# Kernel tuning notes

Hardware: AMD Instinct MI355X
Metric: run time of the kernel (lower is better)

The kernel has to match this reference:

```python
import jax, jax.numpy as jnp
import numpy as np

# dims: B batch, R seq_num (MSA rows), L seq_len (residues), D emb_dim, C n_emb_2D, H heads
B, R, L, D, C, H = 1, 256, 384, 512, 256, 4
HD = D // H
SCALE = np.float32((HD ** -0.5) / np.sqrt(L))  # head-dim scaling * seqlen_scaling (1/sqrt(L))
EPS = 1e-5


def setup_inputs() -> dict:
    key = jax.random.key(0)
    ks = jax.random.split(key, 6)
    s = 0.02
    return {
        "x": jax.random.normal(ks[0], (B, R, L, D), jnp.float32),
        "pair_feat": jax.random.normal(ks[1], (B, L, L, C), jnp.float32),
        "attn_mask": jnp.ones((B, L), jnp.int32),
        "ln_msa_g": jnp.ones((D,), jnp.float32),
        "ln_msa_b": jnp.zeros((D,), jnp.float32),
        "ln_pair_g": jnp.ones((C,), jnp.float32),
        "ln_pair_b": jnp.zeros((C,), jnp.float32),
        "W_pair": jax.random.normal(ks[2], (C, H), jnp.float32) * s,  # stacked per-head [C,1] linears
        "W_v": jax.random.normal(ks[3], (D, D), jnp.float32) * s,     # stacked per-head [D,HD] value proj
        "W_out": jax.random.normal(ks[4], (D, D), jnp.float32) * s,   # to_out (bias=False)
    }


def _ln(x, g, b):
    mu = jnp.mean(x, axis=-1, keepdims=True)
    var = jnp.mean(jnp.square(x - mu), axis=-1, keepdims=True)
    return (x - mu) * jax.lax.rsqrt(var + EPS) * g + b


def reference(x, pair_feat, attn_mask, ln_msa_g, ln_msa_b, ln_pair_g, ln_pair_b, W_pair, W_v, W_out):
    # MHPair_to_MSA.forward (eval mode, dropout=0)
    msa = _ln(x, ln_msa_g, ln_msa_b)                                  # [B,R,L,D]
    pf = (pair_feat + jnp.swapaxes(pair_feat, 1, 2)) * 0.5            # symmetrize
    pf = _ln(pf, ln_pair_g, ln_pair_b)                                # [B,L,L,C]
    # pair-feature-derived attention logits (no QK^T)
    logits = jnp.einsum('bijc,ch->bhij', pf * SCALE, W_pair)          # [B,H,L,L]
    V = jnp.einsum('brld,de->brle', msa, W_v).reshape(B, R, L, H, HD) # [B,R,L,H,HD]
    mask2 = attn_mask[:, :, None] * attn_mask[:, None, :]             # [B,L,L]
    logits = jnp.where(mask2[:, None, :, :] == 0,
                       jnp.finfo(logits.dtype).min, logits)
    attn = jax.nn.softmax(logits, axis=-1)                            # [B,H,L,L]
    out = jnp.einsum('bhij,brjhd->brihd', attn, V).reshape(B, R, L, D)
    out = out @ W_out                                                 # to_out, bias=False
    return x + out                                                    # residual
```

## Files before the change

kernel.cpp:

```cpp
#include <hip/hip_runtime.h>

#define L_   384
#define D_   512
#define C_   256
#define H_   4
#define RR_  256
#define M1_  98304
#define LL2_ 147456
#define NPAIR_BLOCKS 18480
#define NLN_BLOCKS 24576

typedef __bf16 bf16x8 __attribute__((ext_vector_type(8)));
typedef float f32x4 __attribute__((ext_vector_type(4)));

__device__ __forceinline__ unsigned short f2bf_bits(float f) {
  union { float f; unsigned u; } v; v.f = f;
  return (unsigned short)((v.u + 0x7fffu + ((v.u >> 16) & 1u)) >> 16);
}
__device__ __forceinline__ __bf16 f2bf(float f) {
  union { unsigned short s; __bf16 b; } o; o.s = f2bf_bits(f);
  return o.b;
}

__global__ __launch_bounds__(256) void ln_wtrans_kernel(
    const float* __restrict__ x, const float* __restrict__ g,
    const float* __restrict__ b, __bf16* __restrict__ msa,
    const float* __restrict__ Wv, const float* __restrict__ Wo,
    __bf16* __restrict__ WvT, __bf16* __restrict__ WoT) {
  if (blockIdx.x < NLN_BLOCKS) {
    int row = blockIdx.x * 4 + (threadIdx.x >> 6);
    int lane = threadIdx.x & 63;
    const float4* xr = (const float4*)(x + (size_t)row * D_ + lane * 8);
    float4 v0 = xr[0], v1 = xr[1];
    float s1 = v0.x + v0.y + v0.z + v0.w + v1.x + v1.y + v1.z + v1.w;
    float s2 = v0.x * v0.x + v0.y * v0.y + v0.z * v0.z + v0.w * v0.w +
               v1.x * v1.x + v1.y * v1.y + v1.z * v1.z + v1.w * v1.w;
#pragma unroll
    for (int o = 32; o > 0; o >>= 1) {
      s1 += __shfl_xor(s1, o);
      s2 += __shfl_xor(s2, o);
    }
    float mu = s1 * (1.0f / D_);
    float var = s2 * (1.0f / D_) - mu * mu;
    float rs = rsqrtf(var + 1e-5f);
    const float4* gp = (const float4*)(g + lane * 8);
    const float4* bp = (const float4*)(b + lane * 8);
    float4 g0 = gp[0], g1 = gp[1], b0 = bp[0], b1 = bp[1];
    float y[8];
    y[0] = (v0.x - mu) * rs * g0.x + b0.x;
    y[1] = (v0.y - mu) * rs * g0.y + b0.y;
    y[2] = (v0.z - mu) * rs * g0.z + b0.z;
    y[3] = (v0.w - mu) * rs * g0.w + b0.w;
    y[4] = (v1.x - mu) * rs * g1.x + b1.x;
    y[5] = (v1.y - mu) * rs * g1.y + b1.y;
    y[6] = (v1.z - mu) * rs * g1.z + b1.z;
    y[7] = (v1.w - mu) * rs * g1.w + b1.w;
    uint4 pk;
    pk.x = ((unsigned)f2bf_bits(y[1]) << 16) | f2bf_bits(y[0]);
    pk.y = ((unsigned)f2bf_bits(y[3]) << 16) | f2bf_bits(y[2]);
    pk.z = ((unsigned)f2bf_bits(y[5]) << 16) | f2bf_bits(y[4]);
    pk.w = ((unsigned)f2bf_bits(y[7]) << 16) | f2bf_bits(y[6]);
    *(uint4*)(msa + (size_t)row * D_ + lane * 8) = pk;
  } else {
    int id = (blockIdx.x - NLN_BLOCKS) * 256 + threadIdx.x;
    int m = id >> 18;
    int e = (id >> 9) & 511, d = id & 511;
    const float* W = m ? Wo : Wv;
    __bf16* T = m ? WoT : WvT;
    T[(size_t)e * 512 + d] = f2bf(W[(size_t)d * 512 + e]);
  }
}

__global__ __launch_bounds__(256) void pair_logits_kernel(
    const float* __restrict__ pf, const int* __restrict__ mask,
    const float* __restrict__ g, const float* __restrict__ b,
    const float* __restrict__ Wp, float* __restrict__ logits) {
  unsigned wid = blockIdx.x * 4 + (threadIdx.x >> 6);
  int lane = threadIdx.x & 63;
  unsigned a = wid / 385u;
  unsigned c = wid - a * 385u;
  int i, j;
  if (c < 384u - a) { i = a; j = a + c; }
  else { i = 383 - a; j = i + (c - (384 - a)); }

  int c0 = lane * 4;
  float4 p1 = *(const float4*)(pf + ((size_t)i * L_ + j) * C_ + c0);
  float4 p2 = *(const float4*)(pf + ((size_t)j * L_ + i) * C_ + c0);
  float4 v;
  v.x = 0.5f * (p1.x + p2.x); v.y = 0.5f * (p1.y + p2.y);
  v.z = 0.5f * (p1.z + p2.z); v.w = 0.5f * (p1.w + p2.w);
  float s1 = v.x + v.y + v.z + v.w;
  float s2 = v.x * v.x + v.y * v.y + v.z * v.z + v.w * v.w;
#pragma unroll
  for (int o = 32; o > 0; o >>= 1) {
    s1 += __shfl_xor(s1, o);
    s2 += __shfl_xor(s2, o);
  }
  float mu = s1 * (1.0f / C_);
  float var = s2 * (1.0f / C_) - mu * mu;
  float rs = rsqrtf(var + 1e-5f);
  float4 gv = *(const float4*)(g + c0);
  float4 bv = *(const float4*)(b + c0);
  float y0 = (v.x - mu) * rs * gv.x + bv.x;
  float y1 = (v.y - mu) * rs * gv.y + bv.y;
  float y2 = (v.z - mu) * rs * gv.z + bv.z;
  float y3 = (v.w - mu) * rs * gv.w + bv.w;
  const float4* wp = (const float4*)Wp;
  float4 w0 = wp[c0], w1 = wp[c0 + 1], w2 = wp[c0 + 2], w3 = wp[c0 + 3];
  float4 t;
  t.x = y0 * w0.x + y1 * w1.x + y2 * w2.x + y3 * w3.x;
  t.y = y0 * w0.y + y1 * w1.y + y2 * w2.y + y3 * w3.y;
  t.z = y0 * w0.z + y1 * w1.z + y2 * w2.z + y3 * w3.z;
  t.w = y0 * w0.w + y1 * w1.w + y2 * w2.w + y3 * w3.w;
#pragma unroll
  for (int o = 32; o > 0; o >>= 1) {
    t.x += __shfl_xor(t.x, o);
    t.y += __shfl_xor(t.y, o);
    t.z += __shfl_xor(t.z, o);
    t.w += __shfl_xor(t.w, o);
  }
  if (lane < 8) {
    int h = lane & 3;
    int ii = (lane < 4) ? i : j;
    int jj = (lane < 4) ? j : i;
    bool ok = (mask[i] != 0) && (mask[j] != 0);
    const float NEG = -3.402823466e38f;
    const float SCALE = (float)(0.08838834764831845 / 19.595917942265423);
    float th = (h == 0) ? t.x : (h == 1) ? t.y : (h == 2) ? t.z : t.w;
    logits[(size_t)h * LL2_ + (size_t)ii * L_ + jj] = ok ? SCALE * th : NEG;
  }
}

__global__ __launch_bounds__(256) void softmax_kernel(
    const float* __restrict__ logits, __bf16* __restrict__ attn) {
  int wave = threadIdx.x >> 6, lane = threadIdx.x & 63;
  int row = blockIdx.x * 4 + wave;
  const float* lr = logits + (size_t)row * L_;
  float v[6];
#pragma unroll
  for (int t = 0; t < 6; ++t) v[t] = lr[lane + t * 64];
  float mx = v[0];
#pragma unroll
  for (int t = 1; t < 6; ++t) mx = fmaxf(mx, v[t]);
#pragma unroll
  for (int o = 32; o > 0; o >>= 1) mx = fmaxf(mx, __shfl_xor(mx, o));
  float s = 0.f;
#pragma unroll
  for (int t = 0; t < 6; ++t) { v[t] = __expf(v[t] - mx); s += v[t]; }
#pragma unroll
  for (int o = 32; o > 0; o >>= 1) s += __shfl_xor(s, o);
  float inv = 1.0f / s;
  __bf16* ar = attn + (size_t)row * L_;
#pragma unroll
  for (int t = 0; t < 6; ++t) ar[lane + t * 64] = f2bf(v[t] * inv);
}

__device__ __forceinline__ void gload16(const void* g, void* l) {
  __builtin_amdgcn_global_load_lds(
      (const __attribute__((address_space(1))) void*)g,
      (__attribute__((address_space(3))) void*)l, 16, 0, 0);
}

__device__ __forceinline__ unsigned xcd_swz_3072(unsigned bid) {
  return (bid & 7u) * 384u + (bid >> 3);
}
__device__ __forceinline__ unsigned xcd_swz_768(unsigned bid) {
  return (bid & 7u) * 96u + (bid >> 3);
}

template <int NT>
__device__ __forceinline__ void stage_part32(__bf16* s, const __bf16* g, size_t ld) {
  int tid = threadIdx.x;
#pragma unroll
  for (int i = 0; i < 2; ++i) {
    int cid = i * NT + tid;
    int row = cid >> 2, c = cid & 3;
    int cs = c ^ ((row >> 1) & 3);
    gload16(g + (size_t)row * ld + cs * 8, (char*)s + cid * 16);
  }
}

__device__ __forceinline__ bf16x8 frag_ld32(const __bf16* s, int row, int fk) {
  int c = (fk >> 3) ^ ((row >> 1) & 3);
  return *(const bf16x8*)((const char*)s + row * 64 + c * 16);
}

__device__ __forceinline__ void mainloop256_2s(
    const __bf16* __restrict__ A, size_t ldA,
    const __bf16* __restrict__ B, size_t ldB,
    int K, __bf16* lds, f32x4 acc[8][4]) {
  int lane = threadIdx.x & 63, wave = threadIdx.x >> 6;
  int wm = (wave >> 2) * 128, wn = (wave & 3) * 64;
  int fr = lane & 15, fk = (lane >> 4) * 8;
  int nt = K >> 5;
  const int SLOT = 512 * 32;
  stage_part32<512>(lds, A, ldA);
  stage_part32<512>(lds + 256 * 32, B, ldB);
  for (int t = 0; t < nt; ++t) {
    const __bf16* As = lds + (t & 1) * SLOT;
    const __bf16* Bs = As + 256 * 32;
    if (t + 1 < nt) {
      __bf16* d = lds + ((t + 1) & 1) * SLOT;
      stage_part32<512>(d, A + (size_t)(t + 1) * 32, ldA);
      stage_part32<512>(d + 256 * 32, B + (size_t)(t + 1) * 32, ldB);
      asm volatile("s_waitcnt vmcnt(4)" ::: "memory");
    } else {
      asm volatile("s_waitcnt vmcnt(0)" ::: "memory");
    }
    __builtin_amdgcn_s_barrier();
    bf16x8 bfv[4];
#pragma unroll
    for (int ni = 0; ni < 4; ++ni) bfv[ni] = frag_ld32(Bs, wn + ni * 16 + fr, fk);
#pragma unroll
    for (int half = 0; half < 2; ++half) {
      bf16x8 af[4];
#pragma unroll
      for (int mi = 0; mi < 4; ++mi)
        af[mi] = frag_ld32(As, wm + half * 64 + mi * 16 + fr, fk);
      __builtin_amdgcn_s_setprio(1);
#pragma unroll
      for (int mi = 0; mi < 4; ++mi)
#pragma unroll
        for (int ni = 0; ni < 4; ++ni)
          acc[half * 4 + mi][ni] = __builtin_amdgcn_mfma_f32_16x16x32_bf16(
              af[mi], bfv[ni], acc[half * 4 + mi][ni], 0, 0, 0);
      __builtin_amdgcn_s_setprio(0);
    }
  }
}

__device__ __forceinline__ void mainloop128(
    const __bf16* __restrict__ A, size_t ldA,
    const __bf16* __restrict__ B, size_t ldB,
    int K, __bf16* lds, f32x4 acc[4][4]) {
  int lane = threadIdx.x & 63, wave = threadIdx.x >> 6;
  int wm = (wave >> 1) * 64, wn = (wave & 1) * 64;
  int fr = lane & 15, fk = (lane >> 4) * 8;
  int nt = K >> 5;
  const int SLOT = 256 * 32;
#pragma unroll
  for (int t = 0; t < 3; ++t) {
    stage_part32<256>(lds + t * SLOT, A + t * 32, ldA);
    stage_part32<256>(lds + t * SLOT + 128 * 32, B + t * 32, ldB);
  }
  for (int t = 0; t < nt; ++t) {
    int rem = nt - 1 - t;
    if (rem >= 2)      asm volatile("s_waitcnt vmcnt(8)" ::: "memory");
    else if (rem == 1) asm volatile("s_waitcnt vmcnt(4)" ::: "memory");
    else               asm volatile("s_waitcnt vmcnt(0)" ::: "memory");
    __builtin_amdgcn_s_barrier();
    const __bf16* As = lds + (t & 3) * SLOT;
    const __bf16* Bs = As + 128 * 32;
    if (t + 3 < nt) {
      __bf16* d = lds + ((t + 3) & 3) * SLOT;
      stage_part32<256>(d, A + (size_t)(t + 3) * 32, ldA);
      stage_part32<256>(d + 128 * 32, B + (size_t)(t + 3) * 32, ldB);
    }
    bf16x8 bfv[4];
#pragma unroll
    for (int ni = 0; ni < 4; ++ni) bfv[ni] = frag_ld32(Bs, wn + ni * 16 + fr, fk);
#pragma unroll
    for (int half = 0; half < 2; ++half) {
      bf16x8 af[2];
#pragma unroll
      for (int mi = 0; mi < 2; ++mi)
        af[mi] = frag_ld32(As, wm + half * 32 + mi * 16 + fr, fk);
      __builtin_amdgcn_s_setprio(1);
#pragma unroll
      for (int mi = 0; mi < 2; ++mi)
#pragma unroll
        for (int ni = 0; ni < 4; ++ni)
          acc[half * 2 + mi][ni] = __builtin_amdgcn_mfma_f32_16x16x32_bf16(
              af[mi], bfv[ni], acc[half * 2 + mi][ni], 0, 0, 0);
      __builtin_amdgcn_s_setprio(0);
    }
  }
}

__global__ __launch_bounds__(512) void gemm_vt_kernel(
    const __bf16* __restrict__ WvT, const __bf16* __restrict__ msa,
    __bf16* __restrict__ VT) {
  __shared__ __bf16 lds[2 * 512 * 32];
  unsigned swz = xcd_swz_768(blockIdx.x + 2 * blockIdx.y);
  int m0 = (swz & 1) * 256;
  int n0 = (swz >> 1) * 256;
  f32x4 acc[8][4] = {};
  mainloop256_2s(WvT + (size_t)m0 * D_, D_, msa + (size_t)n0 * D_, D_, D_, lds, acc);
  int lane = threadIdx.x & 63, wave = threadIdx.x >> 6;
  int wn = (wave & 3) * 64;
  int cr = (lane >> 4) * 4, cc = lane & 15;
  __bf16* Ep = lds;

  __syncthreads();
#pragma unroll
  for (int p = 0; p < 4; ++p) {
    if ((wave >> 2) == (p >> 1)) {
      int mi0 = (p & 1) * 4;
#pragma unroll
      for (int mi = 0; mi < 4; ++mi)
#pragma unroll
        for (int ni = 0; ni < 4; ++ni)
#pragma unroll
          for (int rr = 0; rr < 4; ++rr) {
            int rowl = mi * 16 + cr + rr;
            int col = wn + ni * 16 + cc;
            int cch = col >> 3;
            Ep[rowl * 256 + (((cch ^ (rowl & 31)) << 3) | (col & 7))] =
                f2bf(acc[mi0 + mi][ni][rr]);
          }
    }
    __syncthreads();
#pragma unroll
    for (int s = 0; s < 4; ++s) {
      int rowl = wave * 8 + s * 2 + (lane >> 5);
      int cch = lane & 31;
      bf16x8 v = *(const bf16x8*)&Ep[rowl * 256 + ((cch ^ (rowl & 31)) << 3)];
      int e = m0 + p * 64 + rowl;
      *(bf16x8*)(VT + (size_t)e * M1_ + n0 + cch * 8) = v;
    }
    __syncthreads();
  }
}

__global__ __launch_bounds__(256) void attnv_kernel(
    const __bf16* __restrict__ attn, const __bf16* __restrict__ VT,
    __bf16* __restrict__ out2) {
  __shared__ __bf16 lds[4 * 256 * 32];
  unsigned swz = xcd_swz_3072(blockIdx.x + 3 * blockIdx.y);
  int it = swz % 3u;
  int rh = swz / 3u;
  int h = rh & 3, r = rh >> 2;
  const __bf16* A = attn + (size_t)h * LL2_ + (size_t)it * 128 * L_;
  const __bf16* Bt = VT + (size_t)(h * 128) * M1_ + (size_t)r * L_;
  f32x4 acc[4][4] = {};
  mainloop128(A, L_, Bt, M1_, L_, lds, acc);
  int lane = threadIdx.x & 63, wave = threadIdx.x >> 6;
  int wm = (wave >> 1) * 64, wn = (wave & 1) * 64;
  int cr = (lane >> 4) * 4, cc = lane & 15;
  __bf16* Ep = lds;

  __syncthreads();
#pragma unroll
  for (int mi = 0; mi < 4; ++mi)
#pragma unroll
    for (int ni = 0; ni < 4; ++ni)
#pragma unroll
      for (int rr = 0; rr < 4; ++rr) {
        int il = wm + mi * 16 + cr + rr;
        int el = wn + ni * 16 + cc;
        int cch = el >> 3;
        Ep[il * 128 + (((cch ^ (il & 15)) << 3) | (el & 7))] =
            f2bf(acc[mi][ni][rr]);
      }
  __syncthreads();
#pragma unroll
  for (int s = 0; s < 8; ++s) {
    int il = wave * 32 + s * 4 + (lane >> 4);
    int cch = lane & 15;
    bf16x8 v = *(const bf16x8*)&Ep[il * 128 + ((cch ^ (il & 15)) << 3)];
    *(bf16x8*)(out2 + ((size_t)(r * L_ + it * 128 + il)) * D_ + h * 128 + cch * 8) = v;
  }
}

__global__ __launch_bounds__(512) void gemm_out_kernel(
    const __bf16* __restrict__ out2, const __bf16* __restrict__ WoT,
    const float* __restrict__ x, float* __restrict__ out) {
  __shared__ __bf16 lds[2 * 512 * 32];
  unsigned swz = xcd_swz_768(blockIdx.x + 2 * blockIdx.y);
  int n0 = (swz & 1) * 256;
  int m0 = (swz >> 1) * 256;
  f32x4 acc[8][4] = {};
  mainloop256_2s(out2 + (size_t)m0 * D_, D_, WoT + (size_t)n0 * D_, D_, D_, lds, acc);
  int lane = threadIdx.x & 63, wave = threadIdx.x >> 6;
  int wn = (wave & 3) * 64;
  int cr = (lane >> 4) * 4, cc = lane & 15;
  float* Ep = (float*)lds;

  __syncthreads();
#pragma unroll
  for (int p = 0; p < 4; ++p) {
    if ((wave >> 2) == (p >> 1)) {
      int mi0 = (p & 1) * 4;
#pragma unroll
      for (int mi = 0; mi < 4; ++mi)
#pragma unroll
        for (int ni = 0; ni < 4; ++ni)
#pragma unroll
          for (int rr = 0; rr < 4; ++rr) {
            int rowl = mi * 16 + cr + rr;
            int col = wn + ni * 16 + cc;
            int c4 = col >> 2;
            Ep[rowl * 256 + (((c4 ^ (rowl & 15)) << 2) | (col & 3))] =
                acc[mi0 + mi][ni][rr];
          }
    }
    __syncthreads();
#pragma unroll
    for (int s = 0; s < 8; ++s) {
      int rowl = wave * 8 + s;
      int grow = m0 + p * 64 + rowl;
      float4 v = *(float4*)&Ep[rowl * 256 + ((lane ^ (rowl & 15)) << 2)];
      float4 xv = *(const float4*)(x + (size_t)grow * D_ + n0 + lane * 4);
      v.x += xv.x; v.y += xv.y; v.z += xv.z; v.w += xv.w;
      *(float4*)(out + (size_t)grow * D_ + n0 + lane * 4) = v;
    }
    __syncthreads();
  }
}

extern "C" void kernel_launch(void* const* d_in, const int* in_sizes, int n_in,
                              void* d_out, int out_size, void* d_ws, size_t ws_size,
                              hipStream_t stream) {
  const float* x      = (const float*)d_in[0];
  const float* pair   = (const float*)d_in[1];
  const int*   mask   = (const int*)d_in[2];
  const float* g_msa  = (const float*)d_in[3];
  const float* b_msa  = (const float*)d_in[4];
  const float* g_pair = (const float*)d_in[5];
  const float* b_pair = (const float*)d_in[6];
  const float* Wp     = (const float*)d_in[7];
  const float* Wv     = (const float*)d_in[8];
  const float* Wo     = (const float*)d_in[9];
  float* out = (float*)d_out;

  char* p = (char*)d_ws;
  auto alloc = [&](size_t bytes) {
    char* r = p;
    p += (bytes + 255) & ~(size_t)255;
    return r;
  };
  __bf16* msa    = (__bf16*)alloc((size_t)M1_ * D_ * 2);
  __bf16* VT     = (__bf16*)alloc((size_t)D_ * M1_ * 2);
  float*  logits = (float*)alloc((size_t)H_ * LL2_ * 4);
  __bf16* attn   = (__bf16*)alloc((size_t)H_ * LL2_ * 2);
  __bf16* WvT    = (__bf16*)alloc((size_t)512 * 512 * 2);
  __bf16* WoT    = (__bf16*)alloc((size_t)512 * 512 * 2);
  __bf16* out2   = msa;

  ln_wtrans_kernel<<<NLN_BLOCKS + 2048, 256, 0, stream>>>(
      x, g_msa, b_msa, msa, Wv, Wo, WvT, WoT);
  gemm_vt_kernel<<<dim3(2, M1_ / 256), 512, 0, stream>>>(WvT, msa, VT);
  pair_logits_kernel<<<NPAIR_BLOCKS, 256, 0, stream>>>(pair, mask, g_pair, b_pair, Wp, logits);
  softmax_kernel<<<(H_ * L_) / 4, 256, 0, stream>>>(logits, attn);
  attnv_kernel<<<dim3(3, RR_ * H_), 256, 0, stream>>>(attn, VT, out2);
  gemm_out_kernel<<<dim3(2, M1_ / 256), 512, 0, stream>>>(out2, WoT, x, out);
}
```

Before: 358.9 us.

## Retile attn-V kernel to cover full 384-row output per block with 512 threads

The attn·V kernel now computes all 384 query rows for one (head, MSA row) pair in a single 512-thread block, rather than splitting them across three 128-row blocks. Each V^T tile is therefore loaded from global memory once instead of three times. The pipeline changes from 4-slot triple-buffered staging to 2-slot double buffering, and the epilogue writes the output in three 128-row passes through LDS. The trade-offs are fewer blocks (1024 vs 3072), more accumulator registers, and less latency hiding from the shallower prefetch.

Result: no change. 364.2 us (+1.5%).

```diff
diff --git a/kernel.cpp b/kernel.cpp
--- a/kernel.cpp
+++ b/kernel.cpp
@@ -161,11 +161,11 @@
       (__attribute__((address_space(3))) void*)l, 16, 0, 0);
 }
 
-__device__ __forceinline__ unsigned xcd_swz_3072(unsigned bid) {
-  return (bid & 7u) * 384u + (bid >> 3);
-}
 __device__ __forceinline__ unsigned xcd_swz_768(unsigned bid) {
   return (bid & 7u) * 96u + (bid >> 3);
+}
+__device__ __forceinline__ unsigned xcd_swz_1024(unsigned bid) {
+  return (bid & 7u) * 128u + (bid >> 3);
 }
 
 template <int NT>
@@ -229,54 +229,6 @@
   }
 }
 
-__device__ __forceinline__ void mainloop128(
-    const __bf16* __restrict__ A, size_t ldA,
-    const __bf16* __restrict__ B, size_t ldB,
-    int K, __bf16* lds, f32x4 acc[4][4]) {
-  int lane = threadIdx.x & 63, wave = threadIdx.x >> 6;
-  int wm = (wave >> 1) * 64, wn = (wave & 1) * 64;
-  int fr = lane & 15, fk = (lane >> 4) * 8;
-  int nt = K >> 5;
-  const int SLOT = 256 * 32;
-#pragma unroll
-  for (int t = 0; t < 3; ++t) {
-    stage_part32<256>(lds + t * SLOT, A + t * 32, ldA);
-    stage_part32<256>(lds + t * SLOT + 128 * 32, B + t * 32, ldB);
-  }
-  for (int t = 0; t < nt; ++t) {
-    int rem = nt - 1 - t;
-    if (rem >= 2)      asm volatile("s_waitcnt vmcnt(8)" ::: "memory");
-    else if (rem == 1) asm volatile("s_waitcnt vmcnt(4)" ::: "memory");
-    else               asm volatile("s_waitcnt vmcnt(0)" ::: "memory");
-    __builtin_amdgcn_s_barrier();
-    const __bf16* As = lds + (t & 3) * SLOT;
-    const __bf16* Bs = As + 128 * 32;
-    if (t + 3 < nt) {
-      __bf16* d = lds + ((t + 3) & 3) * SLOT;
-      stage_part32<256>(d, A + (size_t)(t + 3) * 32, ldA);
-      stage_part32<256>(d + 128 * 32, B + (size_t)(t + 3) * 32, ldB);
-    }
-    bf16x8 bfv[4];
-#pragma unroll
-    for (int ni = 0; ni < 4; ++ni) bfv[ni] = frag_ld32(Bs, wn + ni * 16 + fr, fk);
-#pragma unroll
-    for (int half = 0; half < 2; ++half) {
-      bf16x8 af[2];
-#pragma unroll
-      for (int mi = 0; mi < 2; ++mi)
-        af[mi] = frag_ld32(As, wm + half * 32 + mi * 16 + fr, fk);
-      __builtin_amdgcn_s_setprio(1);
-#pragma unroll
-      for (int mi = 0; mi < 2; ++mi)
-#pragma unroll
-        for (int ni = 0; ni < 4; ++ni)
-          acc[half * 2 + mi][ni] = __builtin_amdgcn_mfma_f32_16x16x32_bf16(
-              af[mi], bfv[ni], acc[half * 2 + mi][ni], 0, 0, 0);
-      __builtin_amdgcn_s_setprio(0);
-    }
-  }
-}
-
 __global__ __launch_bounds__(512) void gemm_vt_kernel(
     const __bf16* __restrict__ WvT, const __bf16* __restrict__ msa,
     __bf16* __restrict__ VT) {
@@ -322,43 +274,99 @@
   }
 }
 
-__global__ __launch_bounds__(256) void attnv_kernel(
+__global__ __launch_bounds__(512) void attnv_kernel(
     const __bf16* __restrict__ attn, const __bf16* __restrict__ VT,
     __bf16* __restrict__ out2) {
-  __shared__ __bf16 lds[4 * 256 * 32];
-  unsigned swz = xcd_swz_3072(blockIdx.x + 3 * blockIdx.y);
-  int it = swz % 3u;
-  int rh = swz / 3u;
-  int h = rh & 3, r = rh >> 2;
-  const __bf16* A = attn + (size_t)h * LL2_ + (size_t)it * 128 * L_;
-  const __bf16* Bt = VT + (size_t)(h * 128) * M1_ + (size_t)r * L_;
-  f32x4 acc[4][4] = {};
-  mainloop128(A, L_, Bt, M1_, L_, lds, acc);
-  int lane = threadIdx.x & 63, wave = threadIdx.x >> 6;
-  int wm = (wave >> 1) * 64, wn = (wave & 1) * 64;
+  __shared__ __bf16 lds[2 * (384 + 128) * 32];
+  unsigned swz = xcd_swz_1024(blockIdx.x);
+  int h = swz >> 8, r = swz & 255;
+  const __bf16* A = attn + (size_t)h * LL2_;
+  const __bf16* B = VT + (size_t)(h * 128) * M1_ + (size_t)r * L_;
+  int tid = threadIdx.x, lane = tid & 63, wave = tid >> 6;
+  int fr = lane & 15, fk = (lane >> 4) * 8;
+  int wm = (wave >> 1) * 96, wn = (wave & 1) * 64;
+  const int SLOT = (384 + 128) * 32;
+
+  auto stage = [&](__bf16* slot, int t) {
+#pragma unroll
+    for (int i = 0; i < 3; ++i) {
+      int cid = i * 512 + tid;
+      int row = cid >> 2, c = cid & 3;
+      int cs = c ^ ((row >> 1) & 3);
+      gload16(A + (size_t)row * L_ + t * 32 + cs * 8, (char*)slot + cid * 16);
+    }
+    {
+      int row = tid >> 2, c = tid & 3;
+      int cs = c ^ ((row >> 1) & 3);
+      gload16(B + (size_t)row * M1_ + t * 32 + cs * 8,
+              (char*)(slot + 384 * 32) + tid * 16);
+    }
+  };
+
+  f32x4 acc[6][4] = {};
+  stage(lds, 0);
+  const int NT = 12;
+  for (int t = 0; t < NT; ++t) {
+    const __bf16* As = lds + (t & 1) * SLOT;
+    const __bf16* Bs = As + 384 * 32;
+    if (t + 1 < NT) {
+      stage(lds + ((t + 1) & 1) * SLOT, t + 1);
+      asm volatile("s_waitcnt vmcnt(4)" ::: "memory");
+    } else {
+      asm volatile("s_waitcnt vmcnt(0)" ::: "memory");
+    }
+    __builtin_amdgcn_s_barrier();
+    bf16x8 bfv[4];
+#pragma unroll
+    for (int ni = 0; ni < 4; ++ni) bfv[ni] = frag_ld32(Bs, wn + ni * 16 + fr, fk);
+#pragma unroll
+    for (int half = 0; half < 2; ++half) {
+      bf16x8 af[3];
+#pragma unroll
+      for (int mi = 0; mi < 3; ++mi)
+        af[mi] = frag_ld32(As, wm + half * 48 + mi * 16 + fr, fk);
+      __builtin_amdgcn_s_setprio(1);
+#pragma unroll
+      for (int mi = 0; mi < 3; ++mi)
+#pragma unroll
+        for (int ni = 0; ni < 4; ++ni)
+          acc[half * 3 + mi][ni] = __builtin_amdgcn_mfma_f32_16x16x32_bf16(
+              af[mi], bfv[ni], acc[half * 3 + mi][ni], 0, 0, 0);
+      __builtin_amdgcn_s_setprio(0);
+    }
+  }
+
   int cr = (lane >> 4) * 4, cc = lane & 15;
   __bf16* Ep = lds;
-
   __syncthreads();
 #pragma unroll
-  for (int mi = 0; mi < 4; ++mi)
-#pragma unroll
-    for (int ni = 0; ni < 4; ++ni)
-#pragma unroll
-      for (int rr = 0; rr < 4; ++rr) {
-        int il = wm + mi * 16 + cr + rr;
-        int el = wn + ni * 16 + cc;
-        int cch = el >> 3;
-        Ep[il * 128 + (((cch ^ (il & 15)) << 3) | (el & 7))] =
-            f2bf(acc[mi][ni][rr]);
+  for (int p = 0; p < 3; ++p) {
+#pragma unroll
+    for (int mi = 0; mi < 6; ++mi) {
+      int gr = wm + mi * 16;
+      if ((gr >> 7) == p) {
+#pragma unroll
+        for (int ni = 0; ni < 4; ++ni)
+#pragma unroll
+          for (int rr = 0; rr < 4; ++rr) {
+            int il = (gr & 127) + cr + rr;
+            int el = wn + ni * 16 + cc;
+            int cch = el >> 3;
+            Ep[il * 128 + (((cch ^ (il & 15)) << 3) | (el & 7))] =
+                f2bf(acc[mi][ni][rr]);
+          }
       }
-  __syncthreads();
-#pragma unroll
-  for (int s = 0; s < 8; ++s) {
-    int il = wave * 32 + s * 4 + (lane >> 4);
-    int cch = lane & 15;
-    bf16x8 v = *(const bf16x8*)&Ep[il * 128 + ((cch ^ (il & 15)) << 3)];
-    *(bf16x8*)(out2 + ((size_t)(r * L_ + it * 128 + il)) * D_ + h * 128 + cch * 8) = v;
+    }
+    __syncthreads();
+#pragma unroll
+    for (int s = 0; s < 4; ++s) {
+      int chunkid = s * 512 + tid;
+      int il = chunkid >> 4, cch = chunkid & 15;
+      bf16x8 v = *(const bf16x8*)&Ep[il * 128 + ((cch ^ (il & 15)) << 3)];
+      int grow = r * L_ + p * 128 + il;
+      *(bf16x8*)(out2 + (size_t)grow * D_ + h * 128 + cch * 8) = v;
+    }
+    __syncthreads();
   }
 }
 
@@ -442,6 +450,6 @@
   gemm_vt_kernel<<<dim3(2, M1_ / 256), 512, 0, stream>>>(WvT, msa, VT);
   pair_logits_kernel<<<NPAIR_BLOCKS, 256, 0, stream>>>(pair, mask, g_pair, b_pair, Wp, logits);
   softmax_kernel<<<(H_ * L_) / 4, 256, 0, stream>>>(logits, attn);
-  attnv_kernel<<<dim3(3, RR_ * H_), 256, 0, stream>>>(attn, VT, out2);
+  attnv_kernel<<<H_ * RR_, 512, 0, stream>>>(attn, VT, out2);
   gemm_out_kernel<<<dim3(2, M1_ / 256), 512, 0, stream>>>(out2, WoT, x, out);
 }
```
